# Optimization experiments

Measured on AMD Instinct MI355X. Metric: run time of the kernel, lower is better.

Reference implementation:

```python
import jax, jax.numpy as jnp
import numpy as np

D_MODEL = 1024
H = 16
T = 1024
B = 8

def setup_inputs() -> dict:
    key = jax.random.key(0)
    k0, k1, k2, k3, k4 = jax.random.split(key, 5)
    return {
        "x": jax.random.normal(k0, (B, T, D_MODEL), dtype=jnp.float32),
        "Wq": jax.random.normal(k1, (D_MODEL, D_MODEL), dtype=jnp.float32),
        "Wk": jax.random.normal(k2, (D_MODEL, D_MODEL), dtype=jnp.float32),
        "Wv": jax.random.normal(k3, (D_MODEL, D_MODEL), dtype=jnp.float32),
        "Wp": jax.random.normal(k4, (D_MODEL, D_MODEL), dtype=jnp.float32),
    }

def reference(x, Wq, Wk, Wv, Wp):
    b, t, d = x.shape
    dh = d // H
    # projections
    q = (x @ Wq).reshape(b, t, H, dh)
    k = (x @ Wk).reshape(b, t, H, dh)
    v = (x @ Wv).reshape(b, t, H, dh)
    # [b, h, t, t] attention scores, scaled by sqrt(d_head)
    scores = jnp.einsum("bqhd,bkhd->bhqk", q, k) / jnp.sqrt(jnp.float32(dh))
    attn = jax.nn.softmax(scores, axis=-1)
    # [b, h, t, dh] -> [b, t, d]
    out = jnp.einsum("bhqk,bkhd->bqhd", attn, v).reshape(b, t, d)
    return out @ Wp
```

## Files before the change

kernel.cpp:

```cpp
#include <hip/hip_runtime.h>
#include <math.h>


typedef unsigned short u16;
typedef unsigned int u32;
typedef __bf16  bf16x8 __attribute__((ext_vector_type(8)));
typedef unsigned short u16x8 __attribute__((ext_vector_type(8)));
typedef unsigned short u16x4 __attribute__((ext_vector_type(4)));
typedef short s16x4 __attribute__((ext_vector_type(4)));
typedef unsigned int u32x2 __attribute__((ext_vector_type(2)));
typedef float f32x4 __attribute__((ext_vector_type(4)));

#define MFMA16(a,b,c) __builtin_amdgcn_mfma_f32_16x16x32_bf16((a),(b),(c),0,0,0)
#define MFMA16K16(a,b,c) __builtin_amdgcn_mfma_f32_16x16x16bf16_1k((a),(b),(c),0,0,0)

static __device__ __forceinline__ u16 f2b(float f){
  unsigned u = __builtin_bit_cast(unsigned, f);
  u += 0x7fffu + ((u >> 16) & 1u);
  return (u16)(u >> 16);
}
static __device__ __forceinline__ float b2f(u16 h){
  unsigned u = ((unsigned)h) << 16;
  return __builtin_bit_cast(float, u);
}
static __device__ __forceinline__ bf16x8 ldsfrag(const u16* p){
  return __builtin_bit_cast(bf16x8, *(const u16x8*)p);
}
static __device__ __forceinline__ u32 packhi(float fa, float fb){
  return __builtin_amdgcn_perm(__builtin_bit_cast(u32, fa),
                               __builtin_bit_cast(u32, fb), 0x07060302u);
}
static __device__ __forceinline__ void gld16(const void* g, void* l){
  __builtin_amdgcn_global_load_lds(
      (const __attribute__((address_space(1))) void*)g,
      (__attribute__((address_space(3))) void*)l, 16, 0, 0);
}


__global__ __launch_bounds__(256) void split_x_kernel(
    const float* __restrict__ x, u16* __restrict__ xh, u16* __restrict__ xl, int n)
{
  int i = (blockIdx.x * 256 + threadIdx.x) * 8;
  if (i >= n) return;
  float4 v0 = *(const float4*)(x + i);
  float4 v1 = *(const float4*)(x + i + 4);
  float vv[8] = {v0.x, v0.y, v0.z, v0.w, v1.x, v1.y, v1.z, v1.w};
  u16x8 hv, lv;
#pragma unroll
  for (int j = 0; j < 8; j++){
    u16 hb = f2b(vv[j]);
    hv[j] = hb;
    lv[j] = f2b(vv[j] - b2f(hb));
  }
  *(u16x8*)(xh + i) = hv;
  *(u16x8*)(xl + i) = lv;
}

__global__ __launch_bounds__(256) void transpose_split_kernel(
    const float* __restrict__ W, u16* __restrict__ Th, u16* __restrict__ Tl,
    int KD, int ND)
{
  __shared__ float t[32][33];
  int n0 = blockIdx.x * 32, k0 = blockIdx.y * 32;
  int tx = threadIdx.x, ty = threadIdx.y;
#pragma unroll
  for (int i = 0; i < 4; i++){
    int k = k0 + ty + i * 8;
    t[ty + i * 8][tx] = W[(size_t)k * ND + n0 + tx];
  }
  __syncthreads();
#pragma unroll
  for (int i = 0; i < 4; i++){
    int n = n0 + ty + i * 8;
    float v = t[tx][ty + i * 8];
    u16 h = f2b(v);
    Th[(size_t)n * KD + k0 + tx] = h;
    if (Tl) Tl[(size_t)n * KD + k0 + tx] = f2b(v - b2f(h));
  }
}

template<int OUTMODE>
__global__ __launch_bounds__(256) void gemm_bt_kernel(
    const u16* __restrict__ A, const u16* __restrict__ Bt, void* __restrict__ Cv,
    int M, int N, int K)
{
  __shared__ __attribute__((aligned(16))) u16 lA[4096], lB[4096];
  const int tid = threadIdx.x, lane = tid & 63, wave = tid >> 6;
  const int quad = lane >> 4, l15 = lane & 15;
  const int row0 = blockIdx.x * 128, col0 = blockIdx.y * 128;
  const int wm = wave >> 1, wn = wave & 1;
  const int sr = lane >> 2, sc = (lane & 3) * 8;
  f32x4 acc[4][4];
#pragma unroll
  for (int mt = 0; mt < 4; mt++)
#pragma unroll
    for (int nt = 0; nt < 4; nt++) acc[mt][nt] = (f32x4)0.0f;

  for (int k0 = 0; k0 < K; k0 += 32){
#pragma unroll
    for (int i = 0; i < 2; i++){
      int c = wave * 2 + i;
      gld16(A  + (size_t)(row0 + c * 16 + sr) * K + k0 + sc, &lA[c * 512]);
      gld16(Bt + (size_t)(col0 + c * 16 + sr) * K + k0 + sc, &lB[c * 512]);
    }
    __syncthreads();
    bf16x8 a[4], b[4];
#pragma unroll
    for (int t = 0; t < 4; t++){
      a[t] = ldsfrag(&lA[(wm * 64 + t * 16 + l15) * 32 + quad * 8]);
      b[t] = ldsfrag(&lB[(wn * 64 + t * 16 + l15) * 32 + quad * 8]);
    }
#pragma unroll
    for (int mt = 0; mt < 4; mt++)
#pragma unroll
      for (int nt = 0; nt < 4; nt++)
        acc[mt][nt] = MFMA16(a[mt], b[nt], acc[mt][nt]);
    __syncthreads();
  }
  if (OUTMODE == 2){
#pragma unroll
    for (int mt = 0; mt < 4; mt++)
#pragma unroll
      for (int nt = 0; nt < 4; nt++){
        int row = row0 + wm * 64 + mt * 16 + quad * 4;
        int col = col0 + wn * 64 + nt * 16 + l15;
        int bb = row >> 10, tt = row & 1023;
        int hh = (col >> 6) & 15, d = col & 63;
        int bhI = bb * 16 + hh;
        int ktile = tt >> 7, fkt = (tt >> 4) & 7, qF = (tt >> 2) & 3;
        int nd = d >> 4, l15F = d & 15;
        size_t idx = ((((size_t)(bhI * 8 + ktile) * 8 + fkt) * 4 + nd) * 64
                      + qF * 16 + l15F) * 4;
        u16x4 vals;
#pragma unroll
        for (int r = 0; r < 4; r++) vals[r] = f2b(acc[mt][nt][r]);
        *(u16x4*)(((u16*)Cv) + idx) = vals;
      }
  } else {
#pragma unroll
    for (int mt = 0; mt < 4; mt++)
#pragma unroll
      for (int nt = 0; nt < 4; nt++)
#pragma unroll
        for (int r = 0; r < 4; r++){
          int row = row0 + wm * 64 + mt * 16 + quad * 4 + r;
          int col = col0 + wn * 64 + nt * 16 + l15;
          ((float*)Cv)[(size_t)row * N + col] = acc[mt][nt][r];
        }
  }
}

__global__ __launch_bounds__(256) void gemm_qk_kernel(
    const u16* __restrict__ Ah, const u16* __restrict__ Al,
    const u16* __restrict__ Bh, const u16* __restrict__ Bl,
    u16* __restrict__ Qhf, u16* __restrict__ Qlf,
    u16* __restrict__ Khf, u16* __restrict__ Klf, int M, int N, int K)
{
  __shared__ __attribute__((aligned(16))) u16 lAh[4096], lAl[4096], lBh[4096], lBl[4096];
  const int tid = threadIdx.x, lane = tid & 63, wave = tid >> 6;
  const int quad = lane >> 4, l15 = lane & 15;
  const int row0 = blockIdx.x * 128, col0 = blockIdx.y * 128;
  const int wm = wave >> 1, wn = wave & 1;
  const int sr = lane >> 2, sc = (lane & 3) * 8;
  f32x4 acc[4][4];
#pragma unroll
  for (int mt = 0; mt < 4; mt++)
#pragma unroll
    for (int nt = 0; nt < 4; nt++) acc[mt][nt] = (f32x4)0.0f;

  for (int k0 = 0; k0 < K; k0 += 32){
#pragma unroll
    for (int i = 0; i < 2; i++){
      int c = wave * 2 + i;
      size_t ao = (size_t)(row0 + c * 16 + sr) * K + k0 + sc;
      size_t bo = (size_t)(col0 + c * 16 + sr) * K + k0 + sc;
      gld16(Ah + ao, &lAh[c * 512]);
      gld16(Al + ao, &lAl[c * 512]);
      gld16(Bh + bo, &lBh[c * 512]);
      gld16(Bl + bo, &lBl[c * 512]);
    }
    __syncthreads();
    bf16x8 ah[4], al[4], bh[4], bl[4];
#pragma unroll
    for (int t = 0; t < 4; t++){
      int aoff = (wm * 64 + t * 16 + l15) * 32 + quad * 8;
      int boff = (wn * 64 + t * 16 + l15) * 32 + quad * 8;
      ah[t] = ldsfrag(&lAh[aoff]);  al[t] = ldsfrag(&lAl[aoff]);
      bh[t] = ldsfrag(&lBh[boff]);  bl[t] = ldsfrag(&lBl[boff]);
    }
#pragma unroll
    for (int mt = 0; mt < 4; mt++)
#pragma unroll
      for (int nt = 0; nt < 4; nt++){
        acc[mt][nt] = MFMA16(al[mt], bh[nt], acc[mt][nt]);
        acc[mt][nt] = MFMA16(ah[mt], bl[nt], acc[mt][nt]);
        acc[mt][nt] = MFMA16(ah[mt], bh[nt], acc[mt][nt]);
      }
    __syncthreads();
  }
  const bool isQ = (col0 < 1024);
#pragma unroll
  for (int mt = 0; mt < 4; mt++)
#pragma unroll
    for (int nt = 0; nt < 4; nt++)
#pragma unroll
      for (int r = 0; r < 4; r++){
        int row = row0 + wm * 64 + mt * 16 + quad * 4 + r;
        int col = col0 + wn * 64 + nt * 16 + l15;
        int bb = row >> 10, tt = row & 1023;
        int hh = (col >> 6) & 15, d = col & 63;
        int bhI = bb * 16 + hh;
        int kc = d >> 5, qF = (d >> 3) & 3, j = d & 7;
        float v = acc[mt][nt][r];
        u16 hi = f2b(v);
        u16 lo = f2b(v - b2f(hi));
        if (isQ){
          int qtile = tt >> 7, rr = tt & 127;
          int wv = rr >> 5, mtF = (rr >> 4) & 1, l15F = tt & 15;
          size_t idx = ((((size_t)(bhI * 8 + qtile) * 4 + wv) * 2 + mtF) * 2 + kc) * 512
                       + (qF * 16 + l15F) * 8 + j;
          Qhf[idx] = hi; Qlf[idx] = lo;
        } else {
          int ktile = tt >> 7, fkt = (tt >> 4) & 7, l15F = tt & 15;
          size_t idx = (((size_t)(bhI * 8 + ktile) * 8 + fkt) * 2 + kc) * 512
                       + (qF * 16 + l15F) * 8 + j;
          Khf[idx] = hi; Klf[idx] = lo;
        }
      }
}

__global__ __launch_bounds__(256, 3) void attn_kernel(
    const u16* __restrict__ Qhf, const u16* __restrict__ Qlf,
    const u16* __restrict__ Khf, const u16* __restrict__ Klf,
    const u16* __restrict__ Vf, u16* __restrict__ O)
{
  __shared__ __attribute__((aligned(16))) u16 lKh[8192], lKl[8192], lV[8192];
  const int tid = threadIdx.x, lane = tid & 63, wave = tid >> 6;
  const int quad = lane >> 4, l15 = lane & 15;
  const int qt = blockIdx.x >> 7, bh = blockIdx.x & 127;
  const int b = bh >> 4, h = bh & 15;
  const int q0 = qt * 128;
  const float BETA = 0.18033688011112042f;

  bf16x8 qh[2][2], ql[2][2];
  {
    size_t qbase = (size_t)(bh * 8 + qt) * 8192 + wave * 2048 + lane * 8;
#pragma unroll
    for (int i = 0; i < 4; i++){
      gld16(Qhf + qbase + i * 512, &lKh[wave * 2048 + i * 512]);
      gld16(Qlf + qbase + i * 512, &lKl[wave * 2048 + i * 512]);
    }
    __syncthreads();
#pragma unroll
    for (int mt = 0; mt < 2; mt++)
#pragma unroll
      for (int kc = 0; kc < 2; kc++){
        int off = wave * 2048 + (mt * 2 + kc) * 512 + lane * 8;
        qh[mt][kc] = ldsfrag(&lKh[off]);
        ql[mt][kc] = ldsfrag(&lKl[off]);
      }
    __syncthreads();
  }

  float m_i[2] = {-3.0e38f, -3.0e38f}, l_i[2] = {0.0f, 0.0f};
  f32x4 o_acc[2][4];
#pragma unroll
  for (int mt = 0; mt < 2; mt++)
#pragma unroll
    for (int nd = 0; nd < 4; nd++) o_acc[mt][nd] = (f32x4)0.0f;

  for (int kt = 0; kt < 8; kt++){
    size_t kbase = (size_t)(bh * 8 + kt) * 8192 + wave * 2048 + lane * 8;
#pragma unroll
    for (int i = 0; i < 4; i++){
      gld16(Khf + kbase + i * 512, &lKh[wave * 2048 + i * 512]);
      gld16(Klf + kbase + i * 512, &lKl[wave * 2048 + i * 512]);
      gld16(Vf  + kbase + i * 512, &lV [wave * 2048 + i * 512]);
    }
    __syncthreads();

#pragma unroll 1
    for (int half = 0; half < 2; half++){
      f32x4 s[2][4];
#pragma unroll
      for (int qt2 = 0; qt2 < 2; qt2++)
#pragma unroll
        for (int f4 = 0; f4 < 4; f4++) s[qt2][f4] = (f32x4)0.0f;
#pragma unroll
      for (int f4 = 0; f4 < 4; f4++){
        int aoff = (half * 4 + f4) * 1024 + lane * 8;
        bf16x8 kh0 = ldsfrag(&lKh[aoff]);
        bf16x8 kh1 = ldsfrag(&lKh[aoff + 512]);
        bf16x8 kl0 = ldsfrag(&lKl[aoff]);
        bf16x8 kl1 = ldsfrag(&lKl[aoff + 512]);
#pragma unroll
        for (int qt2 = 0; qt2 < 2; qt2++){
          s[qt2][f4] = MFMA16(kl0, qh[qt2][0], s[qt2][f4]);
          s[qt2][f4] = MFMA16(kl1, qh[qt2][1], s[qt2][f4]);
          s[qt2][f4] = MFMA16(kh0, ql[qt2][0], s[qt2][f4]);
          s[qt2][f4] = MFMA16(kh1, ql[qt2][1], s[qt2][f4]);
          s[qt2][f4] = MFMA16(kh0, qh[qt2][0], s[qt2][f4]);
          s[qt2][f4] = MFMA16(kh1, qh[qt2][1], s[qt2][f4]);
        }
      }

      float alpha[2];
#pragma unroll
      for (int qt2 = 0; qt2 < 2; qt2++){
        float mx = s[qt2][0][0];
#pragma unroll
        for (int f4 = 0; f4 < 4; f4++)
#pragma unroll
          for (int r = 0; r < 4; r++) mx = fmaxf(mx, s[qt2][f4][r]);
        mx = fmaxf(mx, __shfl_xor(mx, 16));
        mx = fmaxf(mx, __shfl_xor(mx, 32));
        float mn = fmaxf(m_i[qt2], mx);
        alpha[qt2] = __builtin_amdgcn_exp2f((m_i[qt2] - mn) * BETA);
        m_i[qt2] = mn;
        float mb = mn * BETA;
        float rs = 0.0f;
#pragma unroll
        for (int f4 = 0; f4 < 4; f4++)
#pragma unroll
          for (int r = 0; r < 4; r++){
            float p = __builtin_amdgcn_exp2f(s[qt2][f4][r] * BETA - mb);
            s[qt2][f4][r] = p;
            rs += p;
          }
        rs += __shfl_xor(rs, 16);
        rs += __shfl_xor(rs, 32);
        l_i[qt2] = l_i[qt2] * alpha[qt2] + rs;
      }

#pragma unroll
      for (int mt = 0; mt < 2; mt++)
#pragma unroll
        for (int r = 0; r < 4; r++){
          float ar = __shfl(alpha[mt], quad * 4 + r);
#pragma unroll
          for (int nd = 0; nd < 4; nd++) o_acc[mt][nd][r] *= ar;
        }

#pragma unroll
      for (int f4 = 0; f4 < 4; f4++){
        int fkt = half * 4 + f4;
        s16x4 vb[4];
#pragma unroll
        for (int nd = 0; nd < 4; nd++)
          vb[nd] = __builtin_bit_cast(s16x4,
                     *(const u16x4*)&lV[(fkt * 4 + nd) * 256 + lane * 4]);
#pragma unroll
        for (int qt2 = 0; qt2 < 2; qt2++){
          u32x2 pd;
          pd[0] = packhi(s[qt2][f4][1], s[qt2][f4][0]);
          pd[1] = packhi(s[qt2][f4][3], s[qt2][f4][2]);
          s16x4 pa = __builtin_bit_cast(s16x4, pd);
#pragma unroll
          for (int nd = 0; nd < 4; nd++)
            o_acc[qt2][nd] = MFMA16K16(pa, vb[nd], o_acc[qt2][nd]);
        }
      }
    }
    __syncthreads();
  }

#pragma unroll
  for (int mt = 0; mt < 2; mt++)
#pragma unroll
    for (int r = 0; r < 4; r++){
      float lr = __shfl(l_i[mt], quad * 4 + r);
      float inv = 1.0f / lr;
      int t = q0 + wave * 32 + mt * 16 + quad * 4 + r;
      size_t rowoff = (size_t)(b * 1024 + t) * 1024 + h * 64;
#pragma unroll
      for (int nd = 0; nd < 4; nd++)
        O[rowoff + nd * 16 + l15] = f2b(o_acc[mt][nd][r] * inv);
    }
}

extern "C" void kernel_launch(void* const* d_in, const int* in_sizes, int n_in,
                              void* d_out, int out_size, void* d_ws, size_t ws_size,
                              hipStream_t stream)
{
  const float* x  = (const float*)d_in[0];
  const float* Wq = (const float*)d_in[1];
  const float* Wk = (const float*)d_in[2];
  const float* Wv = (const float*)d_in[3];
  const float* Wp = (const float*)d_in[4];
  float* out = (float*)d_out;
  char* ws = (char*)d_ws;
  const size_t MB = 1024 * 1024;
  u16* xh   = (u16*)(ws + 0);
  u16* xl   = (u16*)(ws + 16 * MB);
  u16* wqkh = (u16*)(ws + 32 * MB);
  u16* wqkl = (u16*)(ws + 36 * MB);
  u16* wvt  = (u16*)(ws + 40 * MB);
  u16* wpt  = (u16*)(ws + 42 * MB);
  u16* Qhf  = (u16*)(ws + 44 * MB);
  u16* Qlf  = (u16*)(ws + 60 * MB);
  u16* Khf  = (u16*)(ws + 76 * MB);
  u16* Klf  = (u16*)(ws + 92 * MB);
  u16* Vf   = (u16*)(ws + 108 * MB);
  u16* obuf = xh;
  (void)in_sizes; (void)n_in; (void)out_size; (void)ws_size;

  dim3 tb(32, 8);
  split_x_kernel<<<4096, 256, 0, stream>>>(x, xh, xl, 8 * 1024 * 1024);
  transpose_split_kernel<<<dim3(32, 32), tb, 0, stream>>>(Wq, wqkh, wqkl, 1024, 1024);
  transpose_split_kernel<<<dim3(32, 32), tb, 0, stream>>>(Wk, wqkh + 1024 * 1024, wqkl + 1024 * 1024, 1024, 1024);
  transpose_split_kernel<<<dim3(32, 32), tb, 0, stream>>>(Wv, wvt, (u16*)nullptr, 1024, 1024);
  transpose_split_kernel<<<dim3(32, 32), tb, 0, stream>>>(Wp, wpt, (u16*)nullptr, 1024, 1024);
  gemm_qk_kernel<<<dim3(64, 16), 256, 0, stream>>>(xh, xl, wqkh, wqkl,
                                                   Qhf, Qlf, Khf, Klf, 8192, 2048, 1024);
  gemm_bt_kernel<2><<<dim3(64, 8), 256, 0, stream>>>(xh, wvt, (void*)Vf, 8192, 1024, 1024);
  attn_kernel<<<1024, 256, 0, stream>>>(Qhf, Qlf, Khf, Klf, Vf, obuf);
  gemm_bt_kernel<0><<<dim3(64, 8), 256, 0, stream>>>(obuf, wpt, (void*)out, 8192, 1024, 1024);
}
```

Baseline: 359.0 us.

## Double-buffer K/V tiles in attention and merge four weight transposes into one launch

The attention kernel now streams K/V in 64-key chunks through two LDS buffers, prefetching the next chunk while computing the current one, which removes the load-then-sync stall of each 128-key tile. LDS use stays the same, and there is one barrier per chunk instead of two per tile. The four weight transpose launches are merged into one 3D-grid launch to cut launch overhead. The softmax row max and row sum are also split into partial reductions to shorten dependency chains.

Measured after the change: 355.2 us. No clear change (-1.1%).

```diff
diff --git a/kernel.cpp b/kernel.cpp
--- a/kernel.cpp
+++ b/kernel.cpp
@@ -56,17 +56,24 @@
   *(u16x8*)(xl + i) = lv;
 }
 
-__global__ __launch_bounds__(256) void transpose_split_kernel(
-    const float* __restrict__ W, u16* __restrict__ Th, u16* __restrict__ Tl,
-    int KD, int ND)
+__global__ __launch_bounds__(256) void transpose4_kernel(
+    const float* __restrict__ Wq, const float* __restrict__ Wk,
+    const float* __restrict__ Wv, const float* __restrict__ Wp,
+    u16* __restrict__ qh_, u16* __restrict__ ql_,
+    u16* __restrict__ kh_, u16* __restrict__ kl_,
+    u16* __restrict__ vt_, u16* __restrict__ pt_)
 {
   __shared__ float t[32][33];
+  const int z = blockIdx.z;
+  const float* W = (z == 0) ? Wq : (z == 1) ? Wk : (z == 2) ? Wv : Wp;
+  u16* Th = (z == 0) ? qh_ : (z == 1) ? kh_ : (z == 2) ? vt_ : pt_;
+  u16* Tl = (z == 0) ? ql_ : (z == 1) ? kl_ : nullptr;
   int n0 = blockIdx.x * 32, k0 = blockIdx.y * 32;
   int tx = threadIdx.x, ty = threadIdx.y;
 #pragma unroll
   for (int i = 0; i < 4; i++){
     int k = k0 + ty + i * 8;
-    t[ty + i * 8][tx] = W[(size_t)k * ND + n0 + tx];
+    t[ty + i * 8][tx] = W[(size_t)k * 1024 + n0 + tx];
   }
   __syncthreads();
 #pragma unroll
@@ -74,8 +81,8 @@
     int n = n0 + ty + i * 8;
     float v = t[tx][ty + i * 8];
     u16 h = f2b(v);
-    Th[(size_t)n * KD + k0 + tx] = h;
-    if (Tl) Tl[(size_t)n * KD + k0 + tx] = f2b(v - b2f(h));
+    Th[(size_t)n * 1024 + k0 + tx] = h;
+    if (Tl) Tl[(size_t)n * 1024 + k0 + tx] = f2b(v - b2f(h));
   }
 }
 
@@ -234,7 +241,7 @@
     const u16* __restrict__ Khf, const u16* __restrict__ Klf,
     const u16* __restrict__ Vf, u16* __restrict__ O)
 {
-  __shared__ __attribute__((aligned(16))) u16 lKh[8192], lKl[8192], lV[8192];
+  __shared__ __attribute__((aligned(16))) u16 lKh[2][4096], lKl[2][4096], lV[2][4096];
   const int tid = threadIdx.x, lane = tid & 63, wave = tid >> 6;
   const int quad = lane >> 4, l15 = lane & 15;
   const int qt = blockIdx.x >> 7, bh = blockIdx.x & 127;
@@ -245,10 +252,11 @@
   bf16x8 qh[2][2], ql[2][2];
   {
     size_t qbase = (size_t)(bh * 8 + qt) * 8192 + wave * 2048 + lane * 8;
+    u16* sh = &lKh[0][0];  u16* sl = &lKl[0][0];
 #pragma unroll
     for (int i = 0; i < 4; i++){
-      gld16(Qhf + qbase + i * 512, &lKh[wave * 2048 + i * 512]);
-      gld16(Qlf + qbase + i * 512, &lKl[wave * 2048 + i * 512]);
+      gld16(Qhf + qbase + i * 512, sh + wave * 2048 + i * 512);
+      gld16(Qlf + qbase + i * 512, sl + wave * 2048 + i * 512);
     }
     __syncthreads();
 #pragma unroll
@@ -256,8 +264,8 @@
 #pragma unroll
       for (int kc = 0; kc < 2; kc++){
         int off = wave * 2048 + (mt * 2 + kc) * 512 + lane * 8;
-        qh[mt][kc] = ldsfrag(&lKh[off]);
-        ql[mt][kc] = ldsfrag(&lKl[off]);
+        qh[mt][kc] = ldsfrag(sh + off);
+        ql[mt][kc] = ldsfrag(sl + off);
       }
     __syncthreads();
   }
@@ -269,99 +277,112 @@
 #pragma unroll
     for (int nd = 0; nd < 4; nd++) o_acc[mt][nd] = (f32x4)0.0f;
 
-  for (int kt = 0; kt < 8; kt++){
-    size_t kbase = (size_t)(bh * 8 + kt) * 8192 + wave * 2048 + lane * 8;
-#pragma unroll
-    for (int i = 0; i < 4; i++){
-      gld16(Khf + kbase + i * 512, &lKh[wave * 2048 + i * 512]);
-      gld16(Klf + kbase + i * 512, &lKl[wave * 2048 + i * 512]);
-      gld16(Vf  + kbase + i * 512, &lV [wave * 2048 + i * 512]);
-    }
-    __syncthreads();
+  const size_t pan = (size_t)bh * 65536;
+#pragma unroll
+  for (int i = 0; i < 2; i++){
+    int c = wave * 2 + i;
+    gld16(Khf + pan + c * 512 + lane * 8, &lKh[0][c * 512]);
+    gld16(Klf + pan + c * 512 + lane * 8, &lKl[0][c * 512]);
+    gld16(Vf  + pan + c * 512 + lane * 8, &lV [0][c * 512]);
+  }
 
 #pragma unroll 1
-    for (int half = 0; half < 2; half++){
-      f32x4 s[2][4];
-#pragma unroll
-      for (int qt2 = 0; qt2 < 2; qt2++)
-#pragma unroll
-        for (int f4 = 0; f4 < 4; f4++) s[qt2][f4] = (f32x4)0.0f;
-#pragma unroll
-      for (int f4 = 0; f4 < 4; f4++){
-        int aoff = (half * 4 + f4) * 1024 + lane * 8;
-        bf16x8 kh0 = ldsfrag(&lKh[aoff]);
-        bf16x8 kh1 = ldsfrag(&lKh[aoff + 512]);
-        bf16x8 kl0 = ldsfrag(&lKl[aoff]);
-        bf16x8 kl1 = ldsfrag(&lKl[aoff + 512]);
-#pragma unroll
-        for (int qt2 = 0; qt2 < 2; qt2++){
-          s[qt2][f4] = MFMA16(kl0, qh[qt2][0], s[qt2][f4]);
-          s[qt2][f4] = MFMA16(kl1, qh[qt2][1], s[qt2][f4]);
-          s[qt2][f4] = MFMA16(kh0, ql[qt2][0], s[qt2][f4]);
-          s[qt2][f4] = MFMA16(kh1, ql[qt2][1], s[qt2][f4]);
-          s[qt2][f4] = MFMA16(kh0, qh[qt2][0], s[qt2][f4]);
-          s[qt2][f4] = MFMA16(kh1, qh[qt2][1], s[qt2][f4]);
+  for (int j = 0; j < 16; j++){
+    const int cur = j & 1;
+    __syncthreads();
+    if (j < 15){
+      size_t nb = pan + (size_t)(j + 1) * 4096;
+      const int nxt = cur ^ 1;
+#pragma unroll
+      for (int i = 0; i < 2; i++){
+        int c = wave * 2 + i;
+        gld16(Khf + nb + c * 512 + lane * 8, &lKh[nxt][c * 512]);
+        gld16(Klf + nb + c * 512 + lane * 8, &lKl[nxt][c * 512]);
+        gld16(Vf  + nb + c * 512 + lane * 8, &lV [nxt][c * 512]);
+      }
+    }
+
+    f32x4 s[2][4];
+#pragma unroll
+    for (int qt2 = 0; qt2 < 2; qt2++)
+#pragma unroll
+      for (int f4 = 0; f4 < 4; f4++) s[qt2][f4] = (f32x4)0.0f;
+#pragma unroll
+    for (int f4 = 0; f4 < 4; f4++){
+      int aoff = f4 * 1024 + lane * 8;
+      bf16x8 kh0 = ldsfrag(&lKh[cur][aoff]);
+      bf16x8 kh1 = ldsfrag(&lKh[cur][aoff + 512]);
+      bf16x8 kl0 = ldsfrag(&lKl[cur][aoff]);
+      bf16x8 kl1 = ldsfrag(&lKl[cur][aoff + 512]);
+#pragma unroll
+      for (int qt2 = 0; qt2 < 2; qt2++){
+        s[qt2][f4] = MFMA16(kl0, qh[qt2][0], s[qt2][f4]);
+        s[qt2][f4] = MFMA16(kl1, qh[qt2][1], s[qt2][f4]);
+        s[qt2][f4] = MFMA16(kh0, ql[qt2][0], s[qt2][f4]);
+        s[qt2][f4] = MFMA16(kh1, ql[qt2][1], s[qt2][f4]);
+        s[qt2][f4] = MFMA16(kh0, qh[qt2][0], s[qt2][f4]);
+        s[qt2][f4] = MFMA16(kh1, qh[qt2][1], s[qt2][f4]);
+      }
+    }
+
+    float alpha[2];
+#pragma unroll
+    for (int qt2 = 0; qt2 < 2; qt2++){
+      f32x4 mv = s[qt2][0];
+#pragma unroll
+      for (int f4 = 1; f4 < 4; f4++){
+        mv[0] = fmaxf(mv[0], s[qt2][f4][0]); mv[1] = fmaxf(mv[1], s[qt2][f4][1]);
+        mv[2] = fmaxf(mv[2], s[qt2][f4][2]); mv[3] = fmaxf(mv[3], s[qt2][f4][3]);
+      }
+      float mx = fmaxf(fmaxf(mv[0], mv[1]), fmaxf(mv[2], mv[3]));
+      mx = fmaxf(mx, __shfl_xor(mx, 16));
+      mx = fmaxf(mx, __shfl_xor(mx, 32));
+      float mn = fmaxf(m_i[qt2], mx);
+      alpha[qt2] = __builtin_amdgcn_exp2f((m_i[qt2] - mn) * BETA);
+      m_i[qt2] = mn;
+      float mb = mn * BETA;
+      f32x4 ps = (f32x4)0.0f;
+#pragma unroll
+      for (int f4 = 0; f4 < 4; f4++)
+#pragma unroll
+        for (int r = 0; r < 4; r++){
+          float p = __builtin_amdgcn_exp2f(s[qt2][f4][r] * BETA - mb);
+          s[qt2][f4][r] = p;
+          ps[r] += p;
         }
-      }
-
-      float alpha[2];
+      float rs = (ps[0] + ps[1]) + (ps[2] + ps[3]);
+      rs += __shfl_xor(rs, 16);
+      rs += __shfl_xor(rs, 32);
+      l_i[qt2] = l_i[qt2] * alpha[qt2] + rs;
+    }
+
+#pragma unroll
+    for (int mt = 0; mt < 2; mt++)
+#pragma unroll
+      for (int r = 0; r < 4; r++){
+        float ar = __shfl(alpha[mt], quad * 4 + r);
+#pragma unroll
+        for (int nd = 0; nd < 4; nd++) o_acc[mt][nd][r] *= ar;
+      }
+
+#pragma unroll
+    for (int f4 = 0; f4 < 4; f4++){
+      s16x4 vb[4];
+#pragma unroll
+      for (int nd = 0; nd < 4; nd++)
+        vb[nd] = __builtin_bit_cast(s16x4,
+                   *(const u16x4*)&lV[cur][(f4 * 4 + nd) * 256 + lane * 4]);
 #pragma unroll
       for (int qt2 = 0; qt2 < 2; qt2++){
-        float mx = s[qt2][0][0];
-#pragma unroll
-        for (int f4 = 0; f4 < 4; f4++)
-#pragma unroll
-          for (int r = 0; r < 4; r++) mx = fmaxf(mx, s[qt2][f4][r]);
-        mx = fmaxf(mx, __shfl_xor(mx, 16));
-        mx = fmaxf(mx, __shfl_xor(mx, 32));
-        float mn = fmaxf(m_i[qt2], mx);
-        alpha[qt2] = __builtin_amdgcn_exp2f((m_i[qt2] - mn) * BETA);
-        m_i[qt2] = mn;
-        float mb = mn * BETA;
-        float rs = 0.0f;
-#pragma unroll
-        for (int f4 = 0; f4 < 4; f4++)
-#pragma unroll
-          for (int r = 0; r < 4; r++){
-            float p = __builtin_amdgcn_exp2f(s[qt2][f4][r] * BETA - mb);
-            s[qt2][f4][r] = p;
-            rs += p;
-          }
-        rs += __shfl_xor(rs, 16);
-        rs += __shfl_xor(rs, 32);
-        l_i[qt2] = l_i[qt2] * alpha[qt2] + rs;
-      }
-
-#pragma unroll
-      for (int mt = 0; mt < 2; mt++)
-#pragma unroll
-        for (int r = 0; r < 4; r++){
-          float ar = __shfl(alpha[mt], quad * 4 + r);
-#pragma unroll
-          for (int nd = 0; nd < 4; nd++) o_acc[mt][nd][r] *= ar;
-        }
-
-#pragma unroll
-      for (int f4 = 0; f4 < 4; f4++){
-        int fkt = half * 4 + f4;
-        s16x4 vb[4];
+        u32x2 pd;
+        pd[0] = packhi(s[qt2][f4][1], s[qt2][f4][0]);
+        pd[1] = packhi(s[qt2][f4][3], s[qt2][f4][2]);
+        s16x4 pa = __builtin_bit_cast(s16x4, pd);
 #pragma unroll
         for (int nd = 0; nd < 4; nd++)
-          vb[nd] = __builtin_bit_cast(s16x4,
-                     *(const u16x4*)&lV[(fkt * 4 + nd) * 256 + lane * 4]);
-#pragma unroll
-        for (int qt2 = 0; qt2 < 2; qt2++){
-          u32x2 pd;
-          pd[0] = packhi(s[qt2][f4][1], s[qt2][f4][0]);
-          pd[1] = packhi(s[qt2][f4][3], s[qt2][f4][2]);
-          s16x4 pa = __builtin_bit_cast(s16x4, pd);
-#pragma unroll
-          for (int nd = 0; nd < 4; nd++)
-            o_acc[qt2][nd] = MFMA16K16(pa, vb[nd], o_acc[qt2][nd]);
-        }
-      }
-    }
-    __syncthreads();
+          o_acc[qt2][nd] = MFMA16K16(pa, vb[nd], o_acc[qt2][nd]);
+      }
+    }
   }
 
 #pragma unroll
@@ -404,12 +425,9 @@
   u16* obuf = xh;
   (void)in_sizes; (void)n_in; (void)out_size; (void)ws_size;
 
-  dim3 tb(32, 8);
   split_x_kernel<<<4096, 256, 0, stream>>>(x, xh, xl, 8 * 1024 * 1024);
-  transpose_split_kernel<<<dim3(32, 32), tb, 0, stream>>>(Wq, wqkh, wqkl, 1024, 1024);
-  transpose_split_kernel<<<dim3(32, 32), tb, 0, stream>>>(Wk, wqkh + 1024 * 1024, wqkl + 1024 * 1024, 1024, 1024);
-  transpose_split_kernel<<<dim3(32, 32), tb, 0, stream>>>(Wv, wvt, (u16*)nullptr, 1024, 1024);
-  transpose_split_kernel<<<dim3(32, 32), tb, 0, stream>>>(Wp, wpt, (u16*)nullptr, 1024, 1024);
+  transpose4_kernel<<<dim3(32, 32, 4), dim3(32, 8), 0, stream>>>(
+      Wq, Wk, Wv, Wp, wqkh, wqkl, wqkh + 1024 * 1024, wqkl + 1024 * 1024, wvt, wpt);
   gemm_qk_kernel<<<dim3(64, 16), 256, 0, stream>>>(xh, xl, wqkh, wqkl,
                                                    Qhf, Qlf, Khf, Klf, 8192, 2048, 1024);
   gemm_bt_kernel<2><<<dim3(64, 8), 256, 0, stream>>>(xh, wvt, (void*)Vf, 8192, 1024, 1024);
```
